# Performance work log

Hardware: AMD Instinct MI355X
Metric: run time of the kernel (lower is better)

Reference implementation:

```python
import jax, jax.numpy as jnp
import numpy as np

B, N, D = 64, 32, 512

# Off-diagonal pair indices in the exact order the torch module uses:
# k = N*i + j for i in range(N) for j in range(N) if j != i.
_pairs = [(i, j) for i in range(N) for j in range(N) if j != i]
IDX_I = jnp.asarray(np.array([p[0] for p in _pairs], dtype=np.int32))  # [N*(N-1)]
IDX_J = jnp.asarray(np.array([p[1] for p in _pairs], dtype=np.int32))


def setup_inputs() -> dict:
    key = jax.random.key(0)
    k0, k1, k2 = jax.random.split(key, 3)
    person_feats = jax.random.normal(k0, (B, N, D), dtype=jnp.float32)
    # MLP: Linear(2D -> D) -> ReLU -> Linear(D -> D); Kaiming-ish scaling.
    W1 = jax.random.normal(k1, (D, 2 * D), dtype=jnp.float32) * (1.0 / np.sqrt(2 * D))
    b1 = jnp.zeros((D,), dtype=jnp.float32)
    W2 = jax.random.normal(k2, (D, D), dtype=jnp.float32) * (1.0 / np.sqrt(D))
    b2 = jnp.zeros((D,), dtype=jnp.float32)
    return {"person_feats": person_feats, "W1": W1, "b1": b1, "W2": W2, "b2": b2}


def reference(person_feats, W1, b1, W2, b2):
    # Original math: tem1[b, N*i+j] = feats[b, i]; tem2[b, N*i+j] = feats[b, j];
    # select off-diagonal indices -> pairwise concat(feat_i, feat_j).
    # We gather the N*(N-1) needed pairs directly instead of materializing N*N.
    fi = person_feats[:, IDX_I, :]            # [B, N*(N-1), D]
    fj = person_feats[:, IDX_J, :]            # [B, N*(N-1), D]
    x = jnp.concatenate([fi, fj], axis=-1)    # [B, N*(N-1), 2D]
    h = jax.nn.relu(jnp.einsum('bpk,dk->bpd', x, W1) + b1)
    out = jnp.einsum('bpk,dk->bpd', h, W2) + b2  # [B, N*(N-1), D]
    return out
```

## Files before the change

kernel.cpp:

```cpp
#include <hip/hip_runtime.h>
#include <hip/hip_bf16.h>
#include <stdint.h>


typedef __attribute__((ext_vector_type(4))) float f32x4;
typedef __attribute__((ext_vector_type(8))) short bf16x8;
typedef __attribute__((ext_vector_type(4))) unsigned int u32x4;

__device__ __forceinline__ uint32_t cvt2_bf16(float a, float b) {
    __hip_bfloat162 h = __float22bfloat162_rn(make_float2(a, b));
    uint32_t u;
    __builtin_memcpy(&u, &h, 4);
    return u;
}

__global__ __launch_bounds__(256) void prep(const float* __restrict__ pf,
                                            const float* __restrict__ W1,
                                            const float* __restrict__ b1,
                                            const float* __restrict__ W2,
                                            float* __restrict__ UV,
                                            unsigned short* __restrict__ W2r) {
    __shared__ unsigned short As[32][64];
    __shared__ unsigned short Bs[128][64];

    const int t = threadIdx.x;
    const int bxg = blockIdx.x;

    if (bxg >= 512) {
        int s = (bxg - 512) * 256 + t;
        int l = s & 63;
        int fn = (s >> 6) & 31;
        int kt = s >> 11;
        int col = fn * 16 + (l & 15);
        int k = kt * 32 + (l >> 4) * 8;
        const float* src = W2 + (size_t)col * 512 + k;
        f32x4 a = ((const f32x4*)src)[0];
        f32x4 b = ((const f32x4*)src)[1];
        u32x4 P;
        P[0] = cvt2_bf16(a[0], a[1]); P[1] = cvt2_bf16(a[2], a[3]);
        P[2] = cvt2_bf16(b[0], b[1]); P[3] = cvt2_bf16(b[2], b[3]);
        *(u32x4*)(W2r + (size_t)s * 8) = P;
        return;
    }

    const int m0 = (bxg >> 3) * 32;
    const int c0 = (bxg & 7) * 128;

    const int row8 = t >> 3;
    const int g = t & 7;

    const int wave = t >> 6, lane = t & 63;
    const int wr = wave >> 1, wc = wave & 1;
    const int lr = lane & 15, lkq = lane >> 4;
    const int s7 = lr & 7;

    f32x4 acc[4] = {};

    const float* a_src = pf + (size_t)(m0 + row8) * 512 + g * 8;
    const float* b_src[4];
    int wbB[4];
#pragma unroll
    for (int p = 0; p < 4; ++p) {
        int rb = p * 32 + row8;
        int c = c0 + rb;
        int d = c & 511;
        int koff = (c >> 9) * 512;
        b_src[p] = W1 + (size_t)d * 1024 + koff + g * 8;
        wbB[p] = rb * 128 + ((g ^ (rb & 7)) << 4);
    }
    const int wbA = row8 * 128 + ((g ^ (row8 & 7)) << 4);

    for (int kt = 0; kt < 512; kt += 64) {
        {
            const float* gp = a_src + kt;
            f32x4 x0 = ((const f32x4*)gp)[0];
            f32x4 x1 = ((const f32x4*)gp)[1];
            u32x4 P;
            P[0] = cvt2_bf16(x0[0], x0[1]); P[1] = cvt2_bf16(x0[2], x0[3]);
            P[2] = cvt2_bf16(x1[0], x1[1]); P[3] = cvt2_bf16(x1[2], x1[3]);
            *(u32x4*)((char*)&As[0][0] + wbA) = P;
        }
#pragma unroll
        for (int p = 0; p < 4; ++p) {
            const float* gp = b_src[p] + kt;
            f32x4 x0 = ((const f32x4*)gp)[0];
            f32x4 x1 = ((const f32x4*)gp)[1];
            u32x4 P;
            P[0] = cvt2_bf16(x0[0], x0[1]); P[1] = cvt2_bf16(x0[2], x0[3]);
            P[2] = cvt2_bf16(x1[0], x1[1]); P[3] = cvt2_bf16(x1[2], x1[3]);
            *(u32x4*)((char*)&Bs[0][0] + wbB[p]) = P;
        }
        __syncthreads();
#pragma unroll
        for (int kk = 0; kk < 2; ++kk) {
            const int co = (((kk << 2) + lkq) ^ s7) << 3;
            bf16x8 af = *(const bf16x8*)(&As[0][0] + (wr * 16 + lr) * 64 + co);
#pragma unroll
            for (int n = 0; n < 4; ++n) {
                bf16x8 bfr = *(const bf16x8*)(&Bs[0][0] + (wc * 64 + n * 16 + lr) * 64 + co);
                acc[n] = __builtin_amdgcn_mfma_f32_16x16x32_bf16(af, bfr, acc[n], 0, 0, 0);
            }
        }
        __syncthreads();
    }

    const int cr = lane >> 4;
    const int cc = lane & 15;
#pragma unroll
    for (int n = 0; n < 4; ++n) {
        int c = c0 + wc * 64 + n * 16 + cc;
        float bias = (c < 512) ? b1[c] : 0.0f;
        int rowb = m0 + wr * 16 + cr * 4;
#pragma unroll
        for (int r_ = 0; r_ < 4; ++r_)
            UV[(size_t)(rowb + r_) * 1024 + c] = acc[n][r_] + bias;
    }
}

__global__ __launch_bounds__(256, 2) void fused_gemm(const float* __restrict__ UV,
                                                     const unsigned short* __restrict__ W2r,
                                                     const float* __restrict__ b2,
                                                     float* __restrict__ out) {
    __shared__ unsigned char As[2][4096];

    const int t = threadIdx.x;
    const int bx = blockIdx.x;
    const int mt = (bx & 7) * 124 + (bx >> 3);
    const int m0 = mt << 6;

    const int wave = t >> 6, lane = t & 63;

    const int arow = t >> 2;
    const int ks = t & 3;
    const float* uptr;
    const float* vptr;
    {
        int m = m0 + arow;
        int b = m / 992, p = m - b * 992;
        int i = p / 31, r = p - i * 31;
        int j = r + (r >= i ? 1 : 0);
        uptr = UV + (size_t)(b * 32 + i) * 1024 + ks * 8;
        vptr = UV + (size_t)(b * 32 + j) * 1024 + 512 + ks * 8;
    }
    const int awoff = (arow >> 4) * 1024 + (ks * 16 + (arow & 15)) * 16;

    const unsigned char* bsrc = (const unsigned char*)W2r +
                                (size_t)(wave * 8) * 1024 + lane * 16;

    const int cr = lane >> 4;
    const int cc = lane & 15;

    f32x4 acc[8][4] = {};

    f32x4 Pu0, Pu1, Pv0, Pv1;
    f32x4 Qu0, Qu1, Qv0, Qv1;
    bf16x8 Bp[8], Bq[8];

#define LOAD_B(S, DST)                                                         \
    {                                                                          \
        const unsigned char* gb = bsrc + (size_t)(S) * 32768;                  \
        _Pragma("unroll")                                                      \
        for (int n = 0; n < 8; ++n)                                            \
            DST[n] = *(const bf16x8*)(gb + n * 1024);                          \
    }

#define LOAD_UV(S, U0, U1, V0, V1)                                             \
    {                                                                          \
        const float* up = uptr + (S) * 32;                                     \
        const float* vp = vptr + (S) * 32;                                     \
        U0 = ((const f32x4*)up)[0]; U1 = ((const f32x4*)up)[1];                \
        V0 = ((const f32x4*)vp)[0]; V1 = ((const f32x4*)vp)[1];                \
    }

#define BUILD_A(DSTBUF, U0, U1, V0, V1)                                        \
    {                                                                          \
        f32x4 h0, h1;                                                          \
        _Pragma("unroll")                                                      \
        for (int q = 0; q < 4; ++q) {                                          \
            h0[q] = fmaxf(U0[q] + V0[q], 0.0f);                                \
            h1[q] = fmaxf(U1[q] + V1[q], 0.0f);                                \
        }                                                                      \
        u32x4 P;                                                               \
        P[0] = cvt2_bf16(h0[0], h0[1]); P[1] = cvt2_bf16(h0[2], h0[3]);        \
        P[2] = cvt2_bf16(h1[0], h1[1]); P[3] = cvt2_bf16(h1[2], h1[3]);        \
        *(u32x4*)(&As[DSTBUF][0] + awoff) = P;                                 \
    }

#define MFMA_STEP(BUF, BREG)                                                   \
    {                                                                          \
        const unsigned char* aB = &As[BUF][0];                                 \
        bf16x8 af[4];                                                          \
        _Pragma("unroll")                                                      \
        for (int m = 0; m < 4; ++m)                                            \
            af[m] = *(const bf16x8*)(aB + m * 1024 + lane * 16);               \
        __builtin_amdgcn_s_setprio(1);                                         \
        _Pragma("unroll")                                                      \
        for (int n = 0; n < 8; ++n)                                            \
            _Pragma("unroll")                                                  \
            for (int m = 0; m < 4; ++m)                                        \
                acc[n][m] = __builtin_amdgcn_mfma_f32_16x16x32_bf16(           \
                    af[m], BREG[n], acc[n][m], 0, 0, 0);                       \
        __builtin_amdgcn_s_setprio(0);                                         \
    }

#define BARRIER() asm volatile("s_waitcnt lgkmcnt(0)\n\ts_barrier" ::: "memory")

    LOAD_B(0, Bp);
    LOAD_UV(0, Pu0, Pu1, Pv0, Pv1);
    LOAD_UV(1, Qu0, Qu1, Qv0, Qv1);
    BUILD_A(0, Pu0, Pu1, Pv0, Pv1);

#pragma unroll 1
    for (int s2 = 0; s2 < 16; s2 += 2) {
        BARRIER();
        LOAD_B(s2 + 1, Bq);
        if (s2 < 14) LOAD_UV(s2 + 2, Pu0, Pu1, Pv0, Pv1);
        MFMA_STEP(0, Bp);
        BUILD_A(1, Qu0, Qu1, Qv0, Qv1);

        BARRIER();
        if (s2 < 14) LOAD_B(s2 + 2, Bp);
        if (s2 < 14) LOAD_UV(s2 + 3, Qu0, Qu1, Qv0, Qv1);
        MFMA_STEP(1, Bq);
        if (s2 < 14) BUILD_A(0, Pu0, Pu1, Pv0, Pv1);
    }
#undef LOAD_B
#undef LOAD_UV
#undef BUILD_A
#undef MFMA_STEP
#undef BARRIER

#pragma unroll
    for (int n = 0; n < 8; ++n) {
        int col = wave * 128 + n * 16 + cc;
        float bias = b2[col];
#pragma unroll
        for (int m = 0; m < 4; ++m) {
            int rowb = m0 + m * 16 + cr * 4;
#pragma unroll
            for (int r_ = 0; r_ < 4; ++r_)
                out[(size_t)(rowb + r_) * 512 + col] = acc[n][m][r_] + bias;
        }
    }
}

extern "C" void kernel_launch(void* const* d_in, const int* in_sizes, int n_in,
                              void* d_out, int out_size, void* d_ws, size_t ws_size,
                              hipStream_t stream) {
    const float* pf = (const float*)d_in[0];
    const float* W1 = (const float*)d_in[1];
    const float* b1 = (const float*)d_in[2];
    const float* W2 = (const float*)d_in[3];
    const float* b2 = (const float*)d_in[4];
    float* out = (float*)d_out;

    float* UV = (float*)d_ws;
    unsigned short* W2r = (unsigned short*)((char*)d_ws + (size_t)8 * 1024 * 1024);

    prep<<<dim3(640), dim3(256), 0, stream>>>(pf, W1, b1, W2, UV, W2r);
    fused_gemm<<<dim3(992), dim3(256), 0, stream>>>(UV, W2r, b2, out);
}
```

Before: 73.40 us.

## Double M tile to 128 rows with 8 waves sharing W2 fragments

Each block of the second GEMM now holds 128 output rows and 512 threads, arranged as a 2x4 wave grid. Waves in the same column load the same W2 fragments, so there are half as many blocks and less total B traffic per output row. The B register double buffer is replaced by a single buffer that is refilled in place between MFMAs, which cuts register pressure so two 512-thread blocks can fit per CU. The trade-off is a smaller grid of 496 blocks on 256 CUs, shallower B prefetch that can expose global load latency, and twice the LDS per block.

```diff
diff --git a/kernel.cpp b/kernel.cpp
--- a/kernel.cpp
+++ b/kernel.cpp
@@ -117,18 +117,20 @@
     }
 }
 
-__global__ __launch_bounds__(256, 2) void fused_gemm(const float* __restrict__ UV,
+__global__ __launch_bounds__(512, 2) void fused_gemm(const float* __restrict__ UV,
                                                      const unsigned short* __restrict__ W2r,
                                                      const float* __restrict__ b2,
                                                      float* __restrict__ out) {
-    __shared__ unsigned char As[2][4096];
+    __shared__ unsigned char As[2][8192];
 
     const int t = threadIdx.x;
     const int bx = blockIdx.x;
-    const int mt = (bx & 7) * 124 + (bx >> 3);
-    const int m0 = mt << 6;
+    const int mt = (bx & 7) * 62 + (bx >> 3);
+    const int m0 = mt << 7;
 
     const int wave = t >> 6, lane = t & 63;
+    const int wr = wave >> 2;
+    const int wc = wave & 3;
 
     const int arow = t >> 2;
     const int ks = t & 3;
@@ -145,40 +147,30 @@
     const int awoff = (arow >> 4) * 1024 + (ks * 16 + (arow & 15)) * 16;
 
     const unsigned char* bsrc = (const unsigned char*)W2r +
-                                (size_t)(wave * 8) * 1024 + lane * 16;
+                                (size_t)(wc * 8) * 1024 + lane * 16;
 
     const int cr = lane >> 4;
     const int cc = lane & 15;
 
     f32x4 acc[8][4] = {};
-
+    bf16x8 Bf[8];
     f32x4 Pu0, Pu1, Pv0, Pv1;
-    f32x4 Qu0, Qu1, Qv0, Qv1;
-    bf16x8 Bp[8], Bq[8];
-
-#define LOAD_B(S, DST)                                                         \
-    {                                                                          \
-        const unsigned char* gb = bsrc + (size_t)(S) * 32768;                  \
-        _Pragma("unroll")                                                      \
-        for (int n = 0; n < 8; ++n)                                            \
-            DST[n] = *(const bf16x8*)(gb + n * 1024);                          \
-    }
-
-#define LOAD_UV(S, U0, U1, V0, V1)                                             \
+
+#define LOAD_UV(S)                                                             \
     {                                                                          \
         const float* up = uptr + (S) * 32;                                     \
         const float* vp = vptr + (S) * 32;                                     \
-        U0 = ((const f32x4*)up)[0]; U1 = ((const f32x4*)up)[1];                \
-        V0 = ((const f32x4*)vp)[0]; V1 = ((const f32x4*)vp)[1];                \
-    }
-
-#define BUILD_A(DSTBUF, U0, U1, V0, V1)                                        \
+        Pu0 = ((const f32x4*)up)[0]; Pu1 = ((const f32x4*)up)[1];              \
+        Pv0 = ((const f32x4*)vp)[0]; Pv1 = ((const f32x4*)vp)[1];              \
+    }
+
+#define BUILD_A(DSTBUF)                                                        \
     {                                                                          \
         f32x4 h0, h1;                                                          \
         _Pragma("unroll")                                                      \
         for (int q = 0; q < 4; ++q) {                                          \
-            h0[q] = fmaxf(U0[q] + V0[q], 0.0f);                                \
-            h1[q] = fmaxf(U1[q] + V1[q], 0.0f);                                \
+            h0[q] = fmaxf(Pu0[q] + Pv0[q], 0.0f);                              \
+            h1[q] = fmaxf(Pu1[q] + Pv1[q], 0.0f);                              \
         }                                                                      \
         u32x4 P;                                                               \
         P[0] = cvt2_bf16(h0[0], h0[1]); P[1] = cvt2_bf16(h0[2], h0[3]);        \
@@ -186,57 +178,55 @@
         *(u32x4*)(&As[DSTBUF][0] + awoff) = P;                                 \
     }
 
-#define MFMA_STEP(BUF, BREG)                                                   \
-    {                                                                          \
-        const unsigned char* aB = &As[BUF][0];                                 \
-        bf16x8 af[4];                                                          \
-        _Pragma("unroll")                                                      \
-        for (int m = 0; m < 4; ++m)                                            \
-            af[m] = *(const bf16x8*)(aB + m * 1024 + lane * 16);               \
-        __builtin_amdgcn_s_setprio(1);                                         \
-        _Pragma("unroll")                                                      \
-        for (int n = 0; n < 8; ++n)                                            \
-            _Pragma("unroll")                                                  \
-            for (int m = 0; m < 4; ++m)                                        \
-                acc[n][m] = __builtin_amdgcn_mfma_f32_16x16x32_bf16(           \
-                    af[m], BREG[n], acc[n][m], 0, 0, 0);                       \
-        __builtin_amdgcn_s_setprio(0);                                         \
-    }
-
 #define BARRIER() asm volatile("s_waitcnt lgkmcnt(0)\n\ts_barrier" ::: "memory")
 
-    LOAD_B(0, Bp);
-    LOAD_UV(0, Pu0, Pu1, Pv0, Pv1);
-    LOAD_UV(1, Qu0, Qu1, Qv0, Qv1);
-    BUILD_A(0, Pu0, Pu1, Pv0, Pv1);
+    {
+#pragma unroll
+        for (int n = 0; n < 8; ++n)
+            Bf[n] = *(const bf16x8*)(bsrc + n * 1024);
+        LOAD_UV(0);
+        BUILD_A(0);
+    }
 
 #pragma unroll 1
-    for (int s2 = 0; s2 < 16; s2 += 2) {
+    for (int s = 0; s < 16; ++s) {
         BARRIER();
-        LOAD_B(s2 + 1, Bq);
-        if (s2 < 14) LOAD_UV(s2 + 2, Pu0, Pu1, Pv0, Pv1);
-        MFMA_STEP(0, Bp);
-        BUILD_A(1, Qu0, Qu1, Qv0, Qv1);
-
-        BARRIER();
-        if (s2 < 14) LOAD_B(s2 + 2, Bp);
-        if (s2 < 14) LOAD_UV(s2 + 3, Qu0, Qu1, Qv0, Qv1);
-        MFMA_STEP(1, Bq);
-        if (s2 < 14) BUILD_A(0, Pu0, Pu1, Pv0, Pv1);
-    }
-#undef LOAD_B
+        const int buf = s & 1;
+
+        if (s < 15) LOAD_UV(s + 1);
+
+        const unsigned char* aB = &As[buf][0];
+        bf16x8 af[4];
+#pragma unroll
+        for (int m = 0; m < 4; ++m)
+            af[m] = *(const bf16x8*)(aB + (wr * 4 + m) * 1024 + lane * 16);
+
+        const unsigned char* gb = bsrc + (size_t)(s + 1) * 32768;
+        const bool rel = (s < 15);
+        __builtin_amdgcn_s_setprio(1);
+#pragma unroll
+        for (int n = 0; n < 8; ++n) {
+#pragma unroll
+            for (int m = 0; m < 4; ++m)
+                acc[n][m] = __builtin_amdgcn_mfma_f32_16x16x32_bf16(
+                    af[m], Bf[n], acc[n][m], 0, 0, 0);
+            if (rel) Bf[n] = *(const bf16x8*)(gb + n * 1024);
+        }
+        __builtin_amdgcn_s_setprio(0);
+
+        if (s < 15) BUILD_A(buf ^ 1);
+    }
 #undef LOAD_UV
 #undef BUILD_A
-#undef MFMA_STEP
 #undef BARRIER
 
 #pragma unroll
     for (int n = 0; n < 8; ++n) {
-        int col = wave * 128 + n * 16 + cc;
+        int col = wc * 128 + n * 16 + cc;
         float bias = b2[col];
 #pragma unroll
         for (int m = 0; m < 4; ++m) {
-            int rowb = m0 + m * 16 + cr * 4;
+            int rowb = m0 + wr * 64 + m * 16 + cr * 4;
 #pragma unroll
             for (int r_ = 0; r_ < 4; ++r_)
                 out[(size_t)(rowb + r_) * 512 + col] = acc[n][m][r_] + bias;
@@ -258,5 +248,5 @@
     unsigned short* W2r = (unsigned short*)((char*)d_ws + (size_t)8 * 1024 * 1024);
 
     prep<<<dim3(640), dim3(256), 0, stream>>>(pf, W1, b1, W2, UV, W2r);
-    fused_gemm<<<dim3(992), dim3(256), 0, stream>>>(UV, W2r, b2, out);
-}
+    fused_gemm<<<dim3(496), dim3(512), 0, stream>>>(UV, W2r, b2, out);
+}
```

Result: slower. 87.28 us (+18.9%).
